# Kernel optimization log

Hardware: AMD Instinct MI355X
Metric: run time of the kernel (lower is better)

## Reference

```python
import jax, jax.numpy as jnp
import numpy as np

DEPTH = 8                 # tree depth -> 2^DEPTH leaves
INPUT_SIZE = 128
NB_CLASSES = 10
T = 65536                 # number of states in the trajectory (batched)
N_NODES = (1 << DEPTH) - 1   # 255 internal nodes (BFS order)
N_LEAVES = 1 << DEPTH        # 256 leaves
CLASS_REWARD = np.array([-1.0, -0.5, 0.0, 0.5, 1.0, 1.5, 2.0, 2.5, 3.0, 3.5], dtype=np.float32)


def setup_inputs() -> dict:
    key = jax.random.key(0)
    k_x, k_w, k_b, k_beta, k_leaf = jax.random.split(key, 5)
    x = jax.random.normal(k_x, (T, INPUT_SIZE), dtype=jnp.float32)
    # per-node Linear(input_size, 1): weight [N_NODES, INPUT_SIZE], bias [N_NODES]
    bound = 1.0 / np.sqrt(INPUT_SIZE)
    W = jax.random.uniform(k_w, (N_NODES, INPUT_SIZE), jnp.float32, -bound, bound)
    b = jax.random.uniform(k_b, (N_NODES,), jnp.float32, -bound, bound)
    beta = jax.random.uniform(k_beta, (N_NODES,), jnp.float32, 0.0, 1.0)   # torch.rand(1)
    leaf_dist = jax.random.uniform(k_leaf, (N_LEAVES, NB_CLASSES), jnp.float32, 0.0, 1.0)
    class_reward = jnp.asarray(CLASS_REWARD)
    return {"x": x, "W": W, "b": b, "beta": beta,
            "leaf_dist": leaf_dist, "class_reward": class_reward}


def reference(x, W, b, beta, leaf_dist, class_reward):
    # Gate prob at every internal node (BFS order): sigmoid(beta * (x @ w + b))
    # [T, N_NODES]
    p = jax.nn.sigmoid(beta[None, :] * (x @ W.T + b[None, :]))
    Tn = x.shape[0]
    depth = int(np.log2(p.shape[1] + 1))
    # Level-wise path-prob propagation: mu starts at root = 1.
    mu = jnp.ones((Tn, 1), dtype=x.dtype)
    offset = 0
    for d in range(depth):
        n = 1 << d
        p_lvl = p[:, offset:offset + n]                       # [T, n]
        # child[2i] gets p (left), child[2i+1] gets (1-p) (right)
        mu = (mu[:, :, None] * jnp.stack([p_lvl, 1.0 - p_lvl], axis=-1)).reshape(Tn, 2 * n)
        offset += n
    # Leaf class distributions and scalar reward per leaf
    Q = jax.nn.softmax(leaf_dist, axis=1)                     # [L, C]
    r = Q @ class_reward                                      # [L]
    # traj reward = sum over states and leaves of path_prob * leaf_reward
    return jnp.sum(mu @ r)
```

## Files before the change

kernel.cpp:

```cpp
#include <hip/hip_runtime.h>
#include <hip/hip_bf16.h>

#define NIN      128
#define NCLS     10
#define NNODES   255
#define NLEAVES  256
#define TSAMP    65536

#define MBLK     64
#define PITCH    68
#define NBLOCKS  (TSAMP / MBLK)

typedef short bf16x8 __attribute__((ext_vector_type(8)));
typedef float f32x4  __attribute__((ext_vector_type(4)));

#define LDS_FLOATS (256 * PITCH + 256 + 256 + 256 + 8)

__device__ __forceinline__ short f2b(float f) {
    return __builtin_bit_cast(short, __float2bfloat16(f));
}
__device__ __forceinline__ bf16x8 mk8(float4 a, float4 b) {
    bf16x8 r;
    r[0] = f2b(a.x); r[1] = f2b(a.y); r[2] = f2b(a.z); r[3] = f2b(a.w);
    r[4] = f2b(b.x); r[5] = f2b(b.y); r[6] = f2b(b.z); r[7] = f2b(b.w);
    return r;
}

extern "C" __global__ void __launch_bounds__(256, 1)
sdt_mfma(const float* __restrict__ x, const float* __restrict__ W,
         const float* __restrict__ b, const float* __restrict__ beta,
         const float* __restrict__ leaf_dist, const float* __restrict__ cr,
         float* __restrict__ out) {
    extern __shared__ float smem[];
    float* Lg    = smem;
    float* rl    = smem + 256 * PITCH;
    float* bl    = rl + 256;
    float* betal = bl + 256;
    float* red   = betal + 256;

    const int tid  = threadIdx.x;
    const int lane = tid & 63;
    const int w    = tid >> 6;

    if (tid < NNODES) { bl[tid] = b[tid]; betal[tid] = beta[tid]; }
    {
        float v[NCLS]; float mx = -1e30f;
        #pragma unroll
        for (int c = 0; c < NCLS; ++c) { v[c] = leaf_dist[tid * NCLS + c]; mx = fmaxf(mx, v[c]); }
        float s = 0.f, d = 0.f;
        #pragma unroll
        for (int c = 0; c < NCLS; ++c) { float e = __expf(v[c] - mx); s += e; d += e * cr[c]; }
        rl[tid] = __fdividef(d, s);
    }

    const int r16 = lane & 15;
    const int kg  = lane >> 4;
    const int m0  = blockIdx.x * MBLK;
    const int n0  = w * 64;

    f32x4 acc[4][4];
    #pragma unroll
    for (int i = 0; i < 4; ++i) {
        #pragma unroll
        for (int j = 0; j < 4; ++j) acc[i][j] = (f32x4){0.f, 0.f, 0.f, 0.f};
    }

    const float4* ap = (const float4*)(x + (size_t)(m0 + r16) * NIN + kg * 8);
    const float4* bp0; const float4* bp1; const float4* bp2; const float4* bp3;
    {
        int nA = n0 + 0  + r16; if (nA > 254) nA = 254;
        int nB = n0 + 16 + r16; if (nB > 254) nB = 254;
        int nC = n0 + 32 + r16; if (nC > 254) nC = 254;
        int nD = n0 + 48 + r16; if (nD > 254) nD = 254;
        bp0 = (const float4*)(W + (size_t)nA * NIN + kg * 8);
        bp1 = (const float4*)(W + (size_t)nB * NIN + kg * 8);
        bp2 = (const float4*)(W + (size_t)nC * NIN + kg * 8);
        bp3 = (const float4*)(W + (size_t)nD * NIN + kg * 8);
    }

    #pragma unroll
    for (int ks = 0; ks < 4; ++ks) {
        bf16x8 af[4], bfr[4];
        #pragma unroll
        for (int mf = 0; mf < 4; ++mf)
            af[mf] = mk8(ap[mf * 512 + ks * 8], ap[mf * 512 + ks * 8 + 1]);
        bfr[0] = mk8(bp0[ks * 8], bp0[ks * 8 + 1]);
        bfr[1] = mk8(bp1[ks * 8], bp1[ks * 8 + 1]);
        bfr[2] = mk8(bp2[ks * 8], bp2[ks * 8 + 1]);
        bfr[3] = mk8(bp3[ks * 8], bp3[ks * 8 + 1]);
        #pragma unroll
        for (int mf = 0; mf < 4; ++mf) {
            #pragma unroll
            for (int nf = 0; nf < 4; ++nf)
                acc[mf][nf] = __builtin_amdgcn_mfma_f32_16x16x32_bf16(
                    af[mf], bfr[nf], acc[mf][nf], 0, 0, 0);
        }
    }

    #pragma unroll
    for (int mf = 0; mf < 4; ++mf) {
        #pragma unroll
        for (int nf = 0; nf < 4; ++nf) {
            const int node = n0 + nf * 16 + r16;
            const int sl   = mf * 16 + kg * 4;
            *(f32x4*)&Lg[node * PITCH + sl] = acc[mf][nf];
        }
    }
    __syncthreads();

    const int s = lane;
    const int g = w;

    auto PV = [&](int node) -> float {
        float t = betal[node] * (Lg[node * PITCH + s] + bl[node]);
        return __fdividef(1.f, 1.f + __expf(-t));
    };

    float f_pre;
    {
        float pr  = PV(0);
        f_pre = (g & 2) ? (1.f - pr) : pr;
        float p1v = PV(1 + (g >> 1));
        f_pre *= (g & 1) ? (1.f - p1v) : p1v;
    }

    float q0, q1, q2, q3, q4, F0, F1, F2, F3, F4, accv;
    q0 = PV(3 + g);            F0 = f_pre * q0;
    q1 = PV(7 + 2 * g);        F1 = F0 * q1;
    q2 = PV(15 + 4 * g);       F2 = F1 * q2;
    q3 = PV(31 + 8 * g);       F3 = F2 * q3;
    q4 = PV(63 + 16 * g);      F4 = F3 * q4;
    {
        float p7 = PV(127 + 32 * g);
        accv = F4 * (p7 * rl[g * 64] + (1.f - p7) * rl[g * 64 + 1]);
    }
    for (int LL = 2; LL < 64; LL += 2) {
        const int z = __builtin_ctz((unsigned)LL);
        switch (z) {
            case 1:  F4 = F3 * (1.f - q4); break;
            case 2:  F3 = F2 * (1.f - q3); break;
            case 3:  F2 = F1 * (1.f - q2); break;
            case 4:  F1 = F0 * (1.f - q1); break;
            default: F0 = f_pre * (1.f - q0); break;
        }
        if (z >= 5) { q1 = PV(7  + 2 * g  + (LL >> 5)); F1 = F0 * q1; }
        if (z >= 4) { q2 = PV(15 + 4 * g  + (LL >> 4)); F2 = F1 * q2; }
        if (z >= 3) { q3 = PV(31 + 8 * g  + (LL >> 3)); F3 = F2 * q3; }
        if (z >= 2) { q4 = PV(63 + 16 * g + (LL >> 2)); F4 = F3 * q4; }
        float p7 = PV(127 + 32 * g + (LL >> 1));
        accv += F4 * (p7 * rl[g * 64 + LL] + (1.f - p7) * rl[g * 64 + LL + 1]);
    }

    #pragma unroll
    for (int off = 32; off > 0; off >>= 1) accv += __shfl_down(accv, off);
    if (lane == 0) red[w] = accv;
    __syncthreads();
    if (tid == 0) atomicAdd(out, (red[0] + red[1]) + (red[2] + red[3]));
}

extern "C" void kernel_launch(void* const* d_in, const int* in_sizes, int n_in,
                              void* d_out, int out_size, void* d_ws, size_t ws_size,
                              hipStream_t stream) {
    const float* x            = (const float*)d_in[0];
    const float* W            = (const float*)d_in[1];
    const float* b            = (const float*)d_in[2];
    const float* beta         = (const float*)d_in[3];
    const float* leaf_dist    = (const float*)d_in[4];
    const float* class_reward = (const float*)d_in[5];
    float* out = (float*)d_out;

    hipMemsetAsync(d_out, 0, sizeof(float), stream);

    const size_t lds_bytes = LDS_FLOATS * sizeof(float);
    hipFuncSetAttribute(reinterpret_cast<const void*>(sdt_mfma),
                        hipFuncAttributeMaxDynamicSharedMemorySize, (int)lds_bytes);

    sdt_mfma<<<NBLOCKS, 256, lds_bytes, stream>>>(x, W, b, beta, leaf_dist,
                                                  class_reward, out);
}
```

Measured before the change: 132.7 us.

## Precompute bf16 beta-scaled weights in prep kernel and evaluate tree bottom-up

A prep kernel folds beta into W and b, converts W to bf16 once, and precomputes per-leaf-pair reward differences in workspace. The main kernel then loads bf16 weights directly, stores logits to LDS as bf16 with a smaller footprint, and allows more blocks per CU via launch_bounds(256,4). Path probabilities are now reduced bottom-up with fma-based interpolation instead of the top-down serial DFS, which cuts exp/LDS traffic and removes branching. The risks are an extra kernel launch and lower precision in the stored logits.

```diff
diff --git a/kernel.cpp b/kernel.cpp
--- a/kernel.cpp
+++ b/kernel.cpp
@@ -4,20 +4,25 @@
 #define NIN      128
 #define NCLS     10
 #define NNODES   255
-#define NLEAVES  256
 #define TSAMP    65536
 
 #define MBLK     64
-#define PITCH    68
 #define NBLOCKS  (TSAMP / MBLK)
+#define LPITCH   72
 
 typedef short bf16x8 __attribute__((ext_vector_type(8)));
+typedef short short4v __attribute__((ext_vector_type(4)));
 typedef float f32x4  __attribute__((ext_vector_type(4)));
 
-#define LDS_FLOATS (256 * PITCH + 256 + 256 + 256 + 8)
+#define WS_BB  65280
+#define WS_RD  66304
+#define WS_R1  66816
 
 __device__ __forceinline__ short f2b(float f) {
     return __builtin_bit_cast(short, __float2bfloat16(f));
+}
+__device__ __forceinline__ float b2f(short h) {
+    return __builtin_bit_cast(float, ((unsigned)(unsigned short)h) << 16);
 }
 __device__ __forceinline__ bf16x8 mk8(float4 a, float4 b) {
     bf16x8 r;
@@ -26,32 +31,60 @@
     return r;
 }
 
-extern "C" __global__ void __launch_bounds__(256, 1)
-sdt_mfma(const float* __restrict__ x, const float* __restrict__ W,
-         const float* __restrict__ b, const float* __restrict__ beta,
-         const float* __restrict__ leaf_dist, const float* __restrict__ cr,
+extern "C" __global__ void __launch_bounds__(128)
+sdt_prep(const float* __restrict__ W, const float* __restrict__ b,
+         const float* __restrict__ beta, const float* __restrict__ leaf_dist,
+         const float* __restrict__ cr, char* __restrict__ ws) {
+    short* Wbf = (short*)ws;
+    float* bb  = (float*)(ws + WS_BB);
+    float* rd  = (float*)(ws + WS_RD);
+    float* r1  = (float*)(ws + WS_R1);
+    const int n = blockIdx.x;
+    const int t = threadIdx.x;
+    if (n < NNODES) {
+        const float be = beta[n];
+        Wbf[n * NIN + t] = f2b(W[n * NIN + t] * be);
+        if (t == 0) bb[n] = be * b[n];
+    } else {
+        float rv[2];
+        #pragma unroll
+        for (int h = 0; h < 2; ++h) {
+            const float* ld = leaf_dist + (size_t)(2 * t + h) * NCLS;
+            float mx = -1e30f;
+            float v[NCLS];
+            #pragma unroll
+            for (int c = 0; c < NCLS; ++c) { v[c] = ld[c]; mx = fmaxf(mx, v[c]); }
+            float s = 0.f, d = 0.f;
+            #pragma unroll
+            for (int c = 0; c < NCLS; ++c) { float e = __expf(v[c] - mx); s += e; d += e * cr[c]; }
+            rv[h] = __fdividef(d, s);
+        }
+        rd[t] = rv[0] - rv[1];
+        r1[t] = rv[1];
+    }
+}
+
+extern "C" __global__ void __launch_bounds__(256, 4)
+sdt_main(const float* __restrict__ x, const char* __restrict__ ws,
          float* __restrict__ out) {
-    extern __shared__ float smem[];
-    float* Lg    = smem;
-    float* rl    = smem + 256 * PITCH;
-    float* bl    = rl + 256;
-    float* betal = bl + 256;
-    float* red   = betal + 256;
+    __shared__ short Lg[256 * LPITCH];
+    __shared__ float bbS[256];
+    __shared__ float rdS[128];
+    __shared__ float r1S[128];
+    __shared__ float v2S[4 * 64];
+    __shared__ float red[8];
+
+    const short* Wbf  = (const short*)ws;
+    const float* g_bb = (const float*)(ws + WS_BB);
+    const float* g_rd = (const float*)(ws + WS_RD);
+    const float* g_r1 = (const float*)(ws + WS_R1);
 
     const int tid  = threadIdx.x;
     const int lane = tid & 63;
     const int w    = tid >> 6;
 
-    if (tid < NNODES) { bl[tid] = b[tid]; betal[tid] = beta[tid]; }
-    {
-        float v[NCLS]; float mx = -1e30f;
-        #pragma unroll
-        for (int c = 0; c < NCLS; ++c) { v[c] = leaf_dist[tid * NCLS + c]; mx = fmaxf(mx, v[c]); }
-        float s = 0.f, d = 0.f;
-        #pragma unroll
-        for (int c = 0; c < NCLS; ++c) { float e = __expf(v[c] - mx); s += e; d += e * cr[c]; }
-        rl[tid] = __fdividef(d, s);
-    }
+    bbS[tid] = (tid < NNODES) ? g_bb[tid] : 0.f;
+    if (tid < 128) { rdS[tid] = g_rd[tid]; r1S[tid] = g_r1[tid]; }
 
     const int r16 = lane & 15;
     const int kg  = lane >> 4;
@@ -60,22 +93,16 @@
 
     f32x4 acc[4][4];
     #pragma unroll
-    for (int i = 0; i < 4; ++i) {
+    for (int i = 0; i < 4; ++i)
         #pragma unroll
         for (int j = 0; j < 4; ++j) acc[i][j] = (f32x4){0.f, 0.f, 0.f, 0.f};
-    }
 
     const float4* ap = (const float4*)(x + (size_t)(m0 + r16) * NIN + kg * 8);
-    const float4* bp0; const float4* bp1; const float4* bp2; const float4* bp3;
-    {
-        int nA = n0 + 0  + r16; if (nA > 254) nA = 254;
-        int nB = n0 + 16 + r16; if (nB > 254) nB = 254;
-        int nC = n0 + 32 + r16; if (nC > 254) nC = 254;
-        int nD = n0 + 48 + r16; if (nD > 254) nD = 254;
-        bp0 = (const float4*)(W + (size_t)nA * NIN + kg * 8);
-        bp1 = (const float4*)(W + (size_t)nB * NIN + kg * 8);
-        bp2 = (const float4*)(W + (size_t)nC * NIN + kg * 8);
-        bp3 = (const float4*)(W + (size_t)nD * NIN + kg * 8);
+    int nidx[4];
+    #pragma unroll
+    for (int nf = 0; nf < 4; ++nf) {
+        int nn = n0 + nf * 16 + r16;
+        nidx[nf] = (nn > 254) ? 254 : nn;
     }
 
     #pragma unroll
@@ -84,17 +111,15 @@
         #pragma unroll
         for (int mf = 0; mf < 4; ++mf)
             af[mf] = mk8(ap[mf * 512 + ks * 8], ap[mf * 512 + ks * 8 + 1]);
-        bfr[0] = mk8(bp0[ks * 8], bp0[ks * 8 + 1]);
-        bfr[1] = mk8(bp1[ks * 8], bp1[ks * 8 + 1]);
-        bfr[2] = mk8(bp2[ks * 8], bp2[ks * 8 + 1]);
-        bfr[3] = mk8(bp3[ks * 8], bp3[ks * 8 + 1]);
-        #pragma unroll
-        for (int mf = 0; mf < 4; ++mf) {
+        #pragma unroll
+        for (int nf = 0; nf < 4; ++nf)
+            bfr[nf] = *(const bf16x8*)(Wbf + nidx[nf] * NIN + ks * 32 + kg * 8);
+        #pragma unroll
+        for (int mf = 0; mf < 4; ++mf)
             #pragma unroll
             for (int nf = 0; nf < 4; ++nf)
                 acc[mf][nf] = __builtin_amdgcn_mfma_f32_16x16x32_bf16(
                     af[mf], bfr[nf], acc[mf][nf], 0, 0, 0);
-        }
     }
 
     #pragma unroll
@@ -102,8 +127,12 @@
         #pragma unroll
         for (int nf = 0; nf < 4; ++nf) {
             const int node = n0 + nf * 16 + r16;
+            const int nd   = (node > 254) ? 254 : node;
             const int sl   = mf * 16 + kg * 4;
-            *(f32x4*)&Lg[node * PITCH + sl] = acc[mf][nf];
+            short4v hv;
+            hv[0] = f2b(acc[mf][nf][0]); hv[1] = f2b(acc[mf][nf][1]);
+            hv[2] = f2b(acc[mf][nf][2]); hv[3] = f2b(acc[mf][nf][3]);
+            *(short4v*)&Lg[nd * LPITCH + sl] = hv;
         }
     }
     __syncthreads();
@@ -111,51 +140,59 @@
     const int s = lane;
     const int g = w;
 
-    auto PV = [&](int node) -> float {
-        float t = betal[node] * (Lg[node * PITCH + s] + bl[node]);
+    auto SIG = [&](int node, int smp) -> float {
+        float t = b2f(Lg[node * LPITCH + smp]) + bbS[node];
         return __fdividef(1.f, 1.f + __expf(-t));
     };
 
-    float f_pre;
+    float v7[32];
+    #pragma unroll
+    for (int i = 0; i < 32; ++i) {
+        float p = SIG(127 + 32 * g + i, s);
+        v7[i] = fmaf(p, rdS[32 * g + i], r1S[32 * g + i]);
+    }
+    float v6[16];
+    #pragma unroll
+    for (int i = 0; i < 16; ++i) {
+        float p = SIG(63 + 16 * g + i, s);
+        v6[i] = fmaf(p, v7[2 * i] - v7[2 * i + 1], v7[2 * i + 1]);
+    }
+    float v5[8];
+    #pragma unroll
+    for (int i = 0; i < 8; ++i) {
+        float p = SIG(31 + 8 * g + i, s);
+        v5[i] = fmaf(p, v6[2 * i] - v6[2 * i + 1], v6[2 * i + 1]);
+    }
+    float v4[4];
+    #pragma unroll
+    for (int i = 0; i < 4; ++i) {
+        float p = SIG(15 + 4 * g + i, s);
+        v4[i] = fmaf(p, v5[2 * i] - v5[2 * i + 1], v5[2 * i + 1]);
+    }
+    float v3[2];
+    #pragma unroll
+    for (int i = 0; i < 2; ++i) {
+        float p = SIG(7 + 2 * g + i, s);
+        v3[i] = fmaf(p, v4[2 * i] - v4[2 * i + 1], v4[2 * i + 1]);
+    }
     {
-        float pr  = PV(0);
-        f_pre = (g & 2) ? (1.f - pr) : pr;
-        float p1v = PV(1 + (g >> 1));
-        f_pre *= (g & 1) ? (1.f - p1v) : p1v;
-    }
-
-    float q0, q1, q2, q3, q4, F0, F1, F2, F3, F4, accv;
-    q0 = PV(3 + g);            F0 = f_pre * q0;
-    q1 = PV(7 + 2 * g);        F1 = F0 * q1;
-    q2 = PV(15 + 4 * g);       F2 = F1 * q2;
-    q3 = PV(31 + 8 * g);       F3 = F2 * q3;
-    q4 = PV(63 + 16 * g);      F4 = F3 * q4;
-    {
-        float p7 = PV(127 + 32 * g);
-        accv = F4 * (p7 * rl[g * 64] + (1.f - p7) * rl[g * 64 + 1]);
-    }
-    for (int LL = 2; LL < 64; LL += 2) {
-        const int z = __builtin_ctz((unsigned)LL);
-        switch (z) {
-            case 1:  F4 = F3 * (1.f - q4); break;
-            case 2:  F3 = F2 * (1.f - q3); break;
-            case 3:  F2 = F1 * (1.f - q2); break;
-            case 4:  F1 = F0 * (1.f - q1); break;
-            default: F0 = f_pre * (1.f - q0); break;
-        }
-        if (z >= 5) { q1 = PV(7  + 2 * g  + (LL >> 5)); F1 = F0 * q1; }
-        if (z >= 4) { q2 = PV(15 + 4 * g  + (LL >> 4)); F2 = F1 * q2; }
-        if (z >= 3) { q3 = PV(31 + 8 * g  + (LL >> 3)); F3 = F2 * q3; }
-        if (z >= 2) { q4 = PV(63 + 16 * g + (LL >> 2)); F4 = F3 * q4; }
-        float p7 = PV(127 + 32 * g + (LL >> 1));
-        accv += F4 * (p7 * rl[g * 64 + LL] + (1.f - p7) * rl[g * 64 + LL + 1]);
-    }
-
-    #pragma unroll
-    for (int off = 32; off > 0; off >>= 1) accv += __shfl_down(accv, off);
-    if (lane == 0) red[w] = accv;
+        float p = SIG(3 + g, s);
+        v2S[g * 64 + s] = fmaf(p, v3[0] - v3[1], v3[1]);
+    }
     __syncthreads();
-    if (tid == 0) atomicAdd(out, (red[0] + red[1]) + (red[2] + red[3]));
+
+    if (tid < 64) {
+        float p0 = SIG(0, tid);
+        float p1 = SIG(1, tid);
+        float p2 = SIG(2, tid);
+        float L  = fmaf(p1, v2S[0 * 64 + tid] - v2S[1 * 64 + tid], v2S[1 * 64 + tid]);
+        float R  = fmaf(p2, v2S[2 * 64 + tid] - v2S[3 * 64 + tid], v2S[3 * 64 + tid]);
+        float val = fmaf(p0, L - R, R);
+        #pragma unroll
+        for (int off = 32; off > 0; off >>= 1) val += __shfl_down(val, off);
+        if (tid == 0) atomicAdd(out, val);
+    }
+    (void)red;
 }
 
 extern "C" void kernel_launch(void* const* d_in, const int* in_sizes, int n_in,
@@ -171,10 +208,7 @@
 
     hipMemsetAsync(d_out, 0, sizeof(float), stream);
 
-    const size_t lds_bytes = LDS_FLOATS * sizeof(float);
-    hipFuncSetAttribute(reinterpret_cast<const void*>(sdt_mfma),
-                        hipFuncAttributeMaxDynamicSharedMemorySize, (int)lds_bytes);
-
-    sdt_mfma<<<NBLOCKS, 256, lds_bytes, stream>>>(x, W, b, beta, leaf_dist,
-                                                  class_reward, out);
-}
+    sdt_prep<<<256, 128, 0, stream>>>(W, b, beta, leaf_dist, class_reward,
+                                      (char*)d_ws);
+    sdt_main<<<NBLOCKS, 256, 0, stream>>>(x, (const char*)d_ws, out);
+}
```

Result: faster. 118.6 us (-10.6%).
